# Optimization experiments

Hardware: AMD Instinct MI355X
Metric: run time of the kernel (lower is better)

## Reference

```python
import jax, jax.numpy as jnp
import numpy as np

EPS = 1e-8
THRESHOLD_FACTOR = 0.5


def setup_inputs() -> dict:
    key = jax.random.key(0)
    k1, k2, k3 = jax.random.split(key, 3)
    B, S, D_IN, D_OUT = 4, 4096, 2048, 2048
    x = jax.random.normal(k1, (B, S, D_IN), dtype=jnp.float32)
    # kaiming-uniform-like init for weight
    bound = 1.0 / np.sqrt(D_IN)
    weight = jax.random.uniform(k2, (D_OUT, D_IN), dtype=jnp.float32,
                                minval=-np.sqrt(3.0) * bound, maxval=np.sqrt(3.0) * bound)
    row_scale = jnp.ones((D_OUT, 1), dtype=jnp.float32)
    bias = jax.random.uniform(k3, (D_OUT,), dtype=jnp.float32, minval=-bound, maxval=bound)
    g = jnp.ones((D_IN,), dtype=jnp.float32)  # input RMSNorm affine weight
    return {"x": x, "weight": weight, "row_scale": row_scale, "bias": bias, "g": g}


def _rms_norm(v, axis):
    return v * jax.lax.rsqrt(jnp.mean(v * v, axis=axis, keepdims=True) + EPS)


def reference(x, weight, row_scale, bias, g):
    # input RMSNorm with affine scale
    xn = _rms_norm(x, -1) * g  # [B,S,Din]
    # row RMSNorm of weight
    w = _rms_norm(weight, 1)  # [Dout,Din]
    # abs-mean threshold ternary quantization
    abs_mean = jnp.mean(jnp.abs(w), axis=1, keepdims=True)  # [Dout,1]
    mask = (jnp.abs(w) > THRESHOLD_FACTOR * abs_mean).astype(w.dtype)
    w_q = jnp.sign(w) * mask  # ternary {-1,0,1}
    # scaled dequant: per-row abs_mean and learned row_scale
    w_eff = w_q * abs_mean * row_scale  # [Dout,Din]
    out = jnp.einsum('bsd,od->bso', xn, w_eff) + bias
    return out
```

## Files before the change

### kernel.cpp

```cpp
#include <hip/hip_runtime.h>
#include <stdint.h>

#define EPSF 1e-8f

using i32x4 = __attribute__((ext_vector_type(4))) int;

__device__ __forceinline__ float wave_sum(float v) {
#pragma unroll
  for (int off = 32; off > 0; off >>= 1) v += __shfl_down(v, off, 64);
  return v;
}
__device__ __forceinline__ float wave_max(float v) {
#pragma unroll
  for (int off = 32; off > 0; off >>= 1) v = fmaxf(v, __shfl_down(v, off, 64));
  return v;
}

__global__ __launch_bounds__(256) void wquant_kernel(
    const float* __restrict__ w, const float* __restrict__ row_scale,
    signed char* __restrict__ wq, float* __restrict__ scale, int K) {
  const int row = blockIdx.x;
  const int t = threadIdx.x;
  const float* wr = w + (size_t)row * K;
  float4 v0 = reinterpret_cast<const float4*>(wr)[2 * t];
  float4 v1 = reinterpret_cast<const float4*>(wr)[2 * t + 1];
  float f[8] = {v0.x, v0.y, v0.z, v0.w, v1.x, v1.y, v1.z, v1.w};
  float sa = 0.f, sq = 0.f;
#pragma unroll
  for (int i = 0; i < 8; ++i) { sa += fabsf(f[i]); sq += f[i] * f[i]; }
  sa = wave_sum(sa);
  sq = wave_sum(sq);
  __shared__ float smA[4], smQ[4];
  const int wid = t >> 6;
  if ((t & 63) == 0) { smA[wid] = sa; smQ[wid] = sq; }
  __syncthreads();
  const float sumabs = smA[0] + smA[1] + smA[2] + smA[3];
  const float sumsq  = smQ[0] + smQ[1] + smQ[2] + smQ[3];
  const float absmean = sumabs / (float)K;
  const float thr = 0.5f * absmean;
  union { signed char c[8]; uint2 u; } pk;
#pragma unroll
  for (int i = 0; i < 8; ++i)
    pk.c[i] = (fabsf(f[i]) > thr) ? (f[i] > 0.f ? (signed char)1 : (signed char)-1)
                                  : (signed char)0;
  reinterpret_cast<uint2*>(wq + (size_t)row * K)[t] = pk.u;
  if (t == 0)
    scale[row] = absmean * rsqrtf(sumsq / (float)K + EPSF) * row_scale[row];
}

__global__ __launch_bounds__(256) void xnorm_kernel(
    const float* __restrict__ x, const float* __restrict__ g,
    signed char* __restrict__ xq, float* __restrict__ sx, int K) {
  const int row = blockIdx.x;
  const int t = threadIdx.x;
  const float* xr = x + (size_t)row * K;
  float4 v0 = reinterpret_cast<const float4*>(xr)[2 * t];
  float4 v1 = reinterpret_cast<const float4*>(xr)[2 * t + 1];
  float f[8] = {v0.x, v0.y, v0.z, v0.w, v1.x, v1.y, v1.z, v1.w};
  float sq = 0.f;
#pragma unroll
  for (int i = 0; i < 8; ++i) sq += f[i] * f[i];
  sq = wave_sum(sq);
  __shared__ float smQ[4], smM[4];
  const int wid = t >> 6;
  if ((t & 63) == 0) smQ[wid] = sq;
  __syncthreads();
  const float sumsq = smQ[0] + smQ[1] + smQ[2] + smQ[3];
  const float rs = rsqrtf(sumsq / (float)K + EPSF);
  float4 g0 = reinterpret_cast<const float4*>(g)[2 * t];
  float4 g1 = reinterpret_cast<const float4*>(g)[2 * t + 1];
  float gg[8] = {g0.x, g0.y, g0.z, g0.w, g1.x, g1.y, g1.z, g1.w};
  float vv[8]; float am = 0.f;
#pragma unroll
  for (int i = 0; i < 8; ++i) {
    vv[i] = f[i] * rs * gg[i];
    am = fmaxf(am, fabsf(vv[i]));
  }
  am = wave_max(am);
  if ((t & 63) == 0) smM[wid] = am;
  __syncthreads();
  const float amax = fmaxf(fmaxf(smM[0], smM[1]), fmaxf(smM[2], smM[3]));
  const float inv = amax > 0.f ? 127.f / amax : 0.f;
  union { signed char c[8]; uint2 u; } pk;
#pragma unroll
  for (int i = 0; i < 8; ++i)
    pk.c[i] = (signed char)__float2int_rn(vv[i] * inv);
  reinterpret_cast<uint2*>(xq + (size_t)row * K)[t] = pk.u;
  if (t == 0) sx[row] = amax > 0.f ? amax / 127.f : 0.f;
}


#define BAR() do { __builtin_amdgcn_sched_barrier(0); \
                   asm volatile("" ::: "memory"); \
                   __builtin_amdgcn_s_barrier(); \
                   asm volatile("" ::: "memory"); \
                   __builtin_amdgcn_sched_barrier(0); } while (0)
#define VM(n) asm volatile("s_waitcnt vmcnt(" #n ")" ::: "memory")

__global__ __launch_bounds__(512, 2) void gemm_kernel(
    const signed char* __restrict__ A,
    const signed char* __restrict__ B,
    const float* __restrict__ scale, const float* __restrict__ bias,
    const float* __restrict__ sx,
    float* __restrict__ C, int M, int N, int K) {
  __shared__ signed char lds[2][2][2][16384];

  const int tid  = threadIdx.x;
  const int lane = tid & 63;
  const int wid  = tid >> 6;
  const int wm   = wid >> 2;
  const int wn   = wid & 3;
  const int fr   = lane & 15;
  const int kq   = lane >> 4;

  const int nwg = gridDim.x;
  const int cpx = nwg >> 3;
  const int swz = (blockIdx.x & 7) * cpx + (blockIdx.x >> 3);
  const int NBN = N >> 8;
  const int bn = swz % NBN;
  const int bm = swz / NBN;
  const int mBase = bm * 256, nBase = bn * 256;

  const size_t Kb = (size_t)K;

  const int sr = tid >> 3;
  const int gsrc = (tid & 7) ^ (sr & 7);
  const char* Abyte = (const char*)A + (size_t)(mBase + sr) * Kb + gsrc * 16;
  const char* Bbyte = (const char*)B +
      (size_t)(nBase + ((sr >> 5) * 64) + (sr & 31)) * Kb + gsrc * 16;

#define STAGE_A(bufi, h, t) do { \
    __builtin_amdgcn_global_load_lds( \
      (const __attribute__((address_space(1))) void*)(Abyte + (size_t)((h) * 64) * Kb + (size_t)(t) * 128), \
      (__attribute__((address_space(3))) void*)(&lds[bufi][0][h][tid * 16]), 16, 0, 0); \
    __builtin_amdgcn_global_load_lds( \
      (const __attribute__((address_space(1))) void*)(Abyte + (size_t)(128 + (h) * 64) * Kb + (size_t)(t) * 128), \
      (__attribute__((address_space(3))) void*)(&lds[bufi][0][h][8192 + tid * 16]), 16, 0, 0); \
  } while (0)

#define STAGE_B(bufi, h, t) do { \
    __builtin_amdgcn_global_load_lds( \
      (const __attribute__((address_space(1))) void*)(Bbyte + (size_t)((h) * 32) * Kb + (size_t)(t) * 128), \
      (__attribute__((address_space(3))) void*)(&lds[bufi][1][h][tid * 16]), 16, 0, 0); \
    __builtin_amdgcn_global_load_lds( \
      (const __attribute__((address_space(1))) void*)(Bbyte + (size_t)(128 + (h) * 32) * Kb + (size_t)(t) * 128), \
      (__attribute__((address_space(3))) void*)(&lds[bufi][1][h][8192 + tid * 16]), 16, 0, 0); \
  } while (0)

  const int slot0 = ((kq ^ (fr & 7)) << 4);
  const int aRowB = (wm * 64 + fr) * 128;
  const int bRowB = (wn * 32 + fr) * 128;

  i32x4 aF[4][2], bF[4][2];
  i32x4 acc[8][4];
#pragma unroll
  for (int m = 0; m < 8; ++m)
#pragma unroll
    for (int n = 0; n < 4; ++n) acc[m][n] = (i32x4){0, 0, 0, 0};

#define LDA(bufi, mg) do { \
    _Pragma("unroll") for (int mm = 0; mm < 4; ++mm) \
    _Pragma("unroll") for (int s = 0; s < 2; ++s) \
      aF[mm][s] = *(const i32x4*)&lds[bufi][0][mg][ \
          aRowB + mm * 2048 + (slot0 ^ (s << 6))]; \
  } while (0)

#define LDB(bufi, np) do { \
    _Pragma("unroll") for (int nn = 0; nn < 2; ++nn) \
    _Pragma("unroll") for (int s = 0; s < 2; ++s) \
      bF[(np) * 2 + nn][s] = *(const i32x4*)&lds[bufi][1][np][ \
          bRowB + nn * 2048 + (slot0 ^ (s << 6))]; \
  } while (0)

#define MFMA_Q(mg, np) do { \
    __builtin_amdgcn_s_setprio(1); \
    _Pragma("unroll") for (int mm = 0; mm < 4; ++mm) \
    _Pragma("unroll") for (int nn = 0; nn < 2; ++nn) { \
      i32x4 c = acc[(mg) * 4 + mm][(np) * 2 + nn]; \
      c = __builtin_amdgcn_mfma_i32_16x16x64_i8(aF[mm][0], bF[(np) * 2 + nn][0], c, 0, 0, 0); \
      c = __builtin_amdgcn_mfma_i32_16x16x64_i8(aF[mm][1], bF[(np) * 2 + nn][1], c, 0, 0, 0); \
      acc[(mg) * 4 + mm][(np) * 2 + nn] = c; \
    } \
    __builtin_amdgcn_s_setprio(0); } while (0)

  const int crowBase = mBase + wm * 128 + kq * 4;
  const int ccolBase = nBase + wn * 64 + fr;

#define STORE_Q(mg, np) do { \
    float sxq_[4][4]; \
    _Pragma("unroll") for (int mm = 0; mm < 4; ++mm) \
    _Pragma("unroll") for (int r = 0; r < 4; ++r) \
      sxq_[mm][r] = sx[crowBase + ((mg) * 4 + mm) * 16 + r]; \
    _Pragma("unroll") for (int nn = 0; nn < 2; ++nn) { \
      const int gc = ccolBase + ((np) * 2 + nn) * 16; \
      const float sc = scale[gc]; \
      const float bi = bias[gc]; \
      _Pragma("unroll") for (int mm = 0; mm < 4; ++mm) { \
        const int r0 = crowBase + ((mg) * 4 + mm) * 16; \
        _Pragma("unroll") for (int r = 0; r < 4; ++r) \
          C[(size_t)(r0 + r) * (size_t)N + (size_t)gc] = \
              (float)acc[(mg) * 4 + mm][(np) * 2 + nn][r] * (sxq_[mm][r] * sc) + bi; \
      } } } while (0)

  STAGE_A(0, 0, 0); STAGE_B(0, 0, 0);
  STAGE_A(0, 1, 0); STAGE_B(0, 1, 0);
  STAGE_A(1, 0, 1); STAGE_B(1, 0, 1);
  VM(8);
  BAR();

  const int NT = K >> 7;
  for (int i = 0; i < (NT >> 1) - 1; ++i) {
    const int t1  = 2 * i + 1;
    const int tn0 = 2 * i + 2;
    const int tn1 = 2 * i + 3;
    LDA(0, 0); LDB(0, 0); STAGE_A(1, 1, t1); VM(6);
    BAR(); MFMA_Q(0, 0);
    LDB(0, 1); STAGE_B(1, 1, t1);
    BAR(); MFMA_Q(0, 1);
    LDA(0, 1); STAGE_A(0, 0, tn0);
    BAR(); MFMA_Q(1, 0);
    STAGE_B(0, 0, tn0); VM(8);
    BAR(); MFMA_Q(1, 1);
    LDA(1, 0); LDB(1, 0); STAGE_A(0, 1, tn0); VM(6);
    BAR(); MFMA_Q(0, 0);
    LDB(1, 1); STAGE_B(0, 1, tn0);
    BAR(); MFMA_Q(0, 1);
    LDA(1, 1); STAGE_A(1, 0, tn1);
    BAR(); MFMA_Q(1, 0);
    STAGE_B(1, 0, tn1); VM(8);
    BAR(); MFMA_Q(1, 1);
  }

  {
    const int tl = NT - 1;
    LDA(0, 0); LDB(0, 0); STAGE_A(1, 1, tl); VM(6);
    BAR(); MFMA_Q(0, 0);
    LDB(0, 1); STAGE_B(1, 1, tl);
    BAR(); MFMA_Q(0, 1);
    LDA(0, 1);
    BAR(); MFMA_Q(1, 0);
    VM(4);
    BAR(); MFMA_Q(1, 1);
    LDA(1, 0); LDB(1, 0); VM(0);
    BAR(); MFMA_Q(0, 0); STORE_Q(0, 0);
    LDB(1, 1);
    BAR(); MFMA_Q(0, 1); STORE_Q(0, 1);
    LDA(1, 1);
    BAR(); MFMA_Q(1, 0); STORE_Q(1, 0);
    BAR(); MFMA_Q(1, 1); STORE_Q(1, 1);
  }
#undef STAGE_A
#undef STAGE_B
#undef LDA
#undef LDB
#undef MFMA_Q
#undef STORE_Q
}

extern "C" void kernel_launch(void* const* d_in, const int* in_sizes, int n_in,
                              void* d_out, int out_size, void* d_ws, size_t ws_size,
                              hipStream_t stream) {
  const float* x         = (const float*)d_in[0];
  const float* weight    = (const float*)d_in[1];
  const float* row_scale = (const float*)d_in[2];
  const float* bias      = (const float*)d_in[3];
  const float* g         = (const float*)d_in[4];
  float* out = (float*)d_out;

  const int Din  = in_sizes[4];
  const int Dout = in_sizes[3];
  const int Mrows = in_sizes[0] / Din;

  char* ws = (char*)d_ws;
  signed char* wq = (signed char*)ws;
  signed char* xq = (signed char*)(ws + (size_t)Dout * Din);
  float* scale = (float*)(ws + (size_t)Dout * Din + (size_t)Mrows * Din);
  float* sx = scale + Dout;

  wquant_kernel<<<Dout, 256, 0, stream>>>(weight, row_scale, wq, scale, Din);
  xnorm_kernel<<<Mrows, 256, 0, stream>>>(x, g, xq, sx, Din);
  const int grid = (Mrows / 256) * (Dout / 256);
  gemm_kernel<<<grid, 512, 0, stream>>>(xq, wq, scale, bias, sx, out,
                                        Mrows, Dout, Din);
}
```

Before: 114.2 us.

## Fuse weight quantization and input normalization into one wave-per-row prep kernel

Merges the separate weight-ternarization and input RMSNorm/int8 quantization kernels into a single launch in which each 64-lane wave handles a whole row, with the weight rows first and then the input rows. Butterfly xor-shuffle reductions replace the shared-memory and __syncthreads block reductions. This removes one kernel launch and the block-level synchronization. In exchange, each lane now holds 32 floats in registers, and the code contains a leftover empty branch and an unused variable.

```diff
diff --git a/kernel.cpp b/kernel.cpp
--- a/kernel.cpp
+++ b/kernel.cpp
@@ -5,88 +5,97 @@
 
 using i32x4 = __attribute__((ext_vector_type(4))) int;
 
-__device__ __forceinline__ float wave_sum(float v) {
-#pragma unroll
-  for (int off = 32; off > 0; off >>= 1) v += __shfl_down(v, off, 64);
+__device__ __forceinline__ float wave_bsum(float v) {
+#pragma unroll
+  for (int off = 1; off < 64; off <<= 1) v += __shfl_xor(v, off, 64);
   return v;
 }
-__device__ __forceinline__ float wave_max(float v) {
-#pragma unroll
-  for (int off = 32; off > 0; off >>= 1) v = fmaxf(v, __shfl_down(v, off, 64));
+__device__ __forceinline__ float wave_bmax(float v) {
+#pragma unroll
+  for (int off = 1; off < 64; off <<= 1) v = fmaxf(v, __shfl_xor(v, off, 64));
   return v;
 }
 
-__global__ __launch_bounds__(256) void wquant_kernel(
+__global__ __launch_bounds__(256) void prep_kernel(
+    const float* __restrict__ x, const float* __restrict__ g,
     const float* __restrict__ w, const float* __restrict__ row_scale,
-    signed char* __restrict__ wq, float* __restrict__ scale, int K) {
-  const int row = blockIdx.x;
-  const int t = threadIdx.x;
-  const float* wr = w + (size_t)row * K;
-  float4 v0 = reinterpret_cast<const float4*>(wr)[2 * t];
-  float4 v1 = reinterpret_cast<const float4*>(wr)[2 * t + 1];
-  float f[8] = {v0.x, v0.y, v0.z, v0.w, v1.x, v1.y, v1.z, v1.w};
-  float sa = 0.f, sq = 0.f;
-#pragma unroll
-  for (int i = 0; i < 8; ++i) { sa += fabsf(f[i]); sq += f[i] * f[i]; }
-  sa = wave_sum(sa);
-  sq = wave_sum(sq);
-  __shared__ float smA[4], smQ[4];
-  const int wid = t >> 6;
-  if ((t & 63) == 0) { smA[wid] = sa; smQ[wid] = sq; }
-  __syncthreads();
-  const float sumabs = smA[0] + smA[1] + smA[2] + smA[3];
-  const float sumsq  = smQ[0] + smQ[1] + smQ[2] + smQ[3];
-  const float absmean = sumabs / (float)K;
-  const float thr = 0.5f * absmean;
-  union { signed char c[8]; uint2 u; } pk;
-#pragma unroll
-  for (int i = 0; i < 8; ++i)
-    pk.c[i] = (fabsf(f[i]) > thr) ? (f[i] > 0.f ? (signed char)1 : (signed char)-1)
-                                  : (signed char)0;
-  reinterpret_cast<uint2*>(wq + (size_t)row * K)[t] = pk.u;
-  if (t == 0)
-    scale[row] = absmean * rsqrtf(sumsq / (float)K + EPSF) * row_scale[row];
-}
-
-__global__ __launch_bounds__(256) void xnorm_kernel(
-    const float* __restrict__ x, const float* __restrict__ g,
-    signed char* __restrict__ xq, float* __restrict__ sx, int K) {
-  const int row = blockIdx.x;
-  const int t = threadIdx.x;
-  const float* xr = x + (size_t)row * K;
-  float4 v0 = reinterpret_cast<const float4*>(xr)[2 * t];
-  float4 v1 = reinterpret_cast<const float4*>(xr)[2 * t + 1];
-  float f[8] = {v0.x, v0.y, v0.z, v0.w, v1.x, v1.y, v1.z, v1.w};
-  float sq = 0.f;
-#pragma unroll
-  for (int i = 0; i < 8; ++i) sq += f[i] * f[i];
-  sq = wave_sum(sq);
-  __shared__ float smQ[4], smM[4];
-  const int wid = t >> 6;
-  if ((t & 63) == 0) smQ[wid] = sq;
-  __syncthreads();
-  const float sumsq = smQ[0] + smQ[1] + smQ[2] + smQ[3];
-  const float rs = rsqrtf(sumsq / (float)K + EPSF);
-  float4 g0 = reinterpret_cast<const float4*>(g)[2 * t];
-  float4 g1 = reinterpret_cast<const float4*>(g)[2 * t + 1];
-  float gg[8] = {g0.x, g0.y, g0.z, g0.w, g1.x, g1.y, g1.z, g1.w};
-  float vv[8]; float am = 0.f;
-#pragma unroll
-  for (int i = 0; i < 8; ++i) {
-    vv[i] = f[i] * rs * gg[i];
-    am = fmaxf(am, fabsf(vv[i]));
-  }
-  am = wave_max(am);
-  if ((t & 63) == 0) smM[wid] = am;
-  __syncthreads();
-  const float amax = fmaxf(fmaxf(smM[0], smM[1]), fmaxf(smM[2], smM[3]));
-  const float inv = amax > 0.f ? 127.f / amax : 0.f;
-  union { signed char c[8]; uint2 u; } pk;
-#pragma unroll
-  for (int i = 0; i < 8; ++i)
-    pk.c[i] = (signed char)__float2int_rn(vv[i] * inv);
-  reinterpret_cast<uint2*>(xq + (size_t)row * K)[t] = pk.u;
-  if (t == 0) sx[row] = amax > 0.f ? amax / 127.f : 0.f;
+    signed char* __restrict__ xq, float* __restrict__ sx,
+    signed char* __restrict__ wq, float* __restrict__ scale,
+    int K, int Dout) {
+  const int lane = threadIdx.x & 63;
+  const int gw = (blockIdx.x << 2) | (threadIdx.x >> 6);
+  const int nf4 = K >> 2;
+  if (gw < Dout) {
+    const int o = gw;
+    const float* wr = w + (size_t)o * K;
+    float4 v[8];
+#pragma unroll
+    for (int c = 0; c < 8; ++c)
+      v[c] = reinterpret_cast<const float4*>(wr)[c * 64 + lane];
+    float sa = 0.f, sq = 0.f;
+#pragma unroll
+    for (int c = 0; c < 8; ++c) {
+      sa += fabsf(v[c].x) + fabsf(v[c].y) + fabsf(v[c].z) + fabsf(v[c].w);
+      sq += v[c].x * v[c].x + v[c].y * v[c].y + v[c].z * v[c].z + v[c].w * v[c].w;
+    }
+    sa = wave_bsum(sa);
+    sq = wave_bsum(sq);
+    const float absmean = sa / (float)K;
+    const float thr = 0.5f * absmean;
+    unsigned int* wq4 = reinterpret_cast<unsigned int*>(wq + (size_t)o * K);
+#pragma unroll
+    for (int c = 0; c < 8; ++c) {
+      union { signed char b[4]; unsigned int u; } pk;
+      const float f[4] = {v[c].x, v[c].y, v[c].z, v[c].w};
+#pragma unroll
+      for (int j = 0; j < 4; ++j)
+        pk.b[j] = (fabsf(f[j]) > thr)
+                      ? (f[j] > 0.f ? (signed char)1 : (signed char)-1)
+                      : (signed char)0;
+      wq4[c * 64 + lane] = pk.u;
+    }
+    if (lane == 0)
+      scale[o] = absmean * rsqrtf(sq / (float)K + EPSF) * row_scale[o];
+  } else if (gw < Dout + (int)(gridDim.x)) {
+  }
+  if (gw >= Dout) {
+    const int row = gw - Dout;
+    const float* xr = x + (size_t)row * K;
+    float4 v[8];
+#pragma unroll
+    for (int c = 0; c < 8; ++c)
+      v[c] = reinterpret_cast<const float4*>(xr)[c * 64 + lane];
+    float sq = 0.f;
+#pragma unroll
+    for (int c = 0; c < 8; ++c)
+      sq += v[c].x * v[c].x + v[c].y * v[c].y + v[c].z * v[c].z + v[c].w * v[c].w;
+    sq = wave_bsum(sq);
+    const float rs = rsqrtf(sq / (float)K + EPSF);
+    float4 vv[8];
+    float am = 0.f;
+#pragma unroll
+    for (int c = 0; c < 8; ++c) {
+      const float4 gg = reinterpret_cast<const float4*>(g)[c * 64 + lane];
+      vv[c].x = v[c].x * rs * gg.x; vv[c].y = v[c].y * rs * gg.y;
+      vv[c].z = v[c].z * rs * gg.z; vv[c].w = v[c].w * rs * gg.w;
+      am = fmaxf(am, fmaxf(fmaxf(fabsf(vv[c].x), fabsf(vv[c].y)),
+                           fmaxf(fabsf(vv[c].z), fabsf(vv[c].w))));
+    }
+    am = wave_bmax(am);
+    const float inv = am > 0.f ? 127.f / am : 0.f;
+    unsigned int* xq4 = reinterpret_cast<unsigned int*>(xq + (size_t)row * K);
+#pragma unroll
+    for (int c = 0; c < 8; ++c) {
+      union { signed char b[4]; unsigned int u; } pk;
+      pk.b[0] = (signed char)__float2int_rn(vv[c].x * inv);
+      pk.b[1] = (signed char)__float2int_rn(vv[c].y * inv);
+      pk.b[2] = (signed char)__float2int_rn(vv[c].z * inv);
+      pk.b[3] = (signed char)__float2int_rn(vv[c].w * inv);
+      xq4[c * 64 + lane] = pk.u;
+    }
+    if (lane == 0) sx[row] = am > 0.f ? am / 127.f : 0.f;
+  }
+  (void)nf4;
 }
 
 
@@ -277,8 +286,8 @@
   float* scale = (float*)(ws + (size_t)Dout * Din + (size_t)Mrows * Din);
   float* sx = scale + Dout;
 
-  wquant_kernel<<<Dout, 256, 0, stream>>>(weight, row_scale, wq, scale, Din);
-  xnorm_kernel<<<Mrows, 256, 0, stream>>>(x, g, xq, sx, Din);
+  prep_kernel<<<(Dout + Mrows) / 4, 256, 0, stream>>>(
+      x, g, weight, row_scale, xq, sx, wq, scale, Din, Dout);
   const int grid = (Mrows / 256) * (Dout / 256);
   gemm_kernel<<<grid, 512, 0, stream>>>(xq, wq, scale, bias, sx, out,
                                         Mrows, Dout, Din);
```

Result: faster. 111.6 us (-2.3%).
